# Optimization experiments

Hardware: AMD Instinct MI355X
Metric: run time of the kernel (lower is better)

## Reference

```python
import jax, jax.numpy as jnp
import numpy as np

D_MODEL, H, KV, HD = 2048, 32, 8, 64  # head_dim = 64, RoPE half-dim = 32
B, L = 2, 2048
EPS = 1e-06


def apply_rope(t, cos, sin):
    # t: [b,l,h,hd]; cos/sin: [1,l,1,hd//2] (broadcast over batch and heads)
    dim = t.shape[-1] // 2
    cos = cos[..., :dim]
    sin = sin[..., :dim]
    x1, x2 = t[..., :dim], t[..., dim:]
    return jnp.concatenate([x1 * cos - x2 * sin, x2 * cos + x1 * sin], axis=-1)


def setup_inputs() -> dict:
    key = jax.random.key(0)
    ks = jax.random.split(key, 5)
    x = jax.random.normal(ks[0], (B, L, D_MODEL), dtype=jnp.float32)
    # true rotary tables, theta=10000
    half = HD // 2
    inv_freq = 1.0 / (10000.0 ** (jnp.arange(half, dtype=jnp.float32) / half))
    ang = jnp.arange(L, dtype=jnp.float32)[:, None] * inv_freq[None, :]  # [L, half]
    cos = jnp.cos(ang)[None, :, None, :]  # [1,L,1,half]
    sin = jnp.sin(ang)[None, :, None, :]
    s = 0.02
    Wq = jax.random.normal(ks[1], (D_MODEL, D_MODEL), dtype=jnp.float32) * s
    Wk = jax.random.normal(ks[2], (D_MODEL, KV * HD), dtype=jnp.float32) * s
    Wv = jax.random.normal(ks[3], (D_MODEL, KV * HD), dtype=jnp.float32) * s
    Wo = jax.random.normal(ks[4], (D_MODEL, D_MODEL), dtype=jnp.float32) * s
    return {"x": x, "cos": cos, "sin": sin, "Wq": Wq, "Wk": Wk, "Wv": Wv, "Wo": Wo}


def reference(x, cos, sin, Wq, Wk, Wv, Wo):
    b, l, _ = x.shape
    q = (x @ Wq).reshape(b, l, H, HD)
    k = (x @ Wk).reshape(b, l, KV, HD)
    v = (x @ Wv).reshape(b, l, KV, HD)
    q = apply_rope(q, cos, sin)
    k = apply_rope(k, cos[:, :, :KV, :], sin[:, :, :KV, :])
    # QK RMS-norm (qk_norm=True path), done in fp32
    q32 = q.astype(jnp.float32)
    k32 = k.astype(jnp.float32)
    q = (q32 * jax.lax.rsqrt(jnp.mean(jnp.square(q32), axis=-1, keepdims=True) + EPS)).astype(q.dtype)
    k = (k32 * jax.lax.rsqrt(jnp.mean(jnp.square(k32), axis=-1, keepdims=True) + EPS)).astype(k.dtype)
    # GQA: repeat KV heads to match Q heads
    g = H // KV
    k = jnp.repeat(k, g, axis=2)
    v = jnp.repeat(v, g, axis=2)
    scale = jax.lax.rsqrt(jnp.float32(HD))
    scores = jnp.einsum('blhd,bmhd->bhlm', q, k) * scale  # [b,H,L,L]
    causal = jnp.tril(jnp.ones((l, l), dtype=jnp.bool_))[None, None]
    scores = jnp.where(causal, scores, jnp.full_like(scores, -10000.0))
    attn = jax.nn.softmax(scores.astype(jnp.float32), axis=-1).astype(v.dtype)
    out = jnp.einsum('bhql,blhd->bqhd', attn, v).reshape(b, l, D_MODEL)
    return out @ Wo
```

## Files before the change

### kernel.cpp

```cpp
#include <hip/hip_runtime.h>
#include <hip/hip_bf16.h>
#include <cstdint>
#include <cstddef>

#define D_MODEL 2048
#define NH 32
#define NKV 8
#define HD 64
#define BB 2
#define LL 2048
#define EPS 1e-6f
#define MM (BB * LL)
#define QS 3072
#define KO 2048
#define VO 2560

typedef __hip_bfloat16 bf16;
typedef short bf16x8 __attribute__((ext_vector_type(8)));
typedef short s16x4 __attribute__((ext_vector_type(4)));
typedef float f32x4 __attribute__((ext_vector_type(4)));

__device__ inline float4 ld_bf4u(const unsigned short* p) {
  const ushort4 u = *(const ushort4*)p;
  float4 r;
  r.x = __uint_as_float(((unsigned)u.x) << 16);
  r.y = __uint_as_float(((unsigned)u.y) << 16);
  r.z = __uint_as_float(((unsigned)u.z) << 16);
  r.w = __uint_as_float(((unsigned)u.w) << 16);
  return r;
}
__device__ inline float4 ld4_rt(const void* p, size_t i, bool f32) {
  if (f32) return *(const float4*)((const float*)p + i);
  return ld_bf4u((const unsigned short*)p + i);
}
__device__ inline float ld1_rt(const void* p, size_t i, bool f32) {
  if (f32) return ((const float*)p)[i];
  unsigned short u = ((const unsigned short*)p)[i];
  return __uint_as_float(((unsigned)u) << 16);
}
__device__ inline unsigned short f2bf(float f) {
  bf16 h = __float2bfloat16(f);
  return *reinterpret_cast<unsigned short*>(&h);
}
__device__ inline float bfu2f(unsigned short u) {
  return __uint_as_float(((unsigned)u) << 16);
}
__device__ inline void store1(float* p, float v) { *p = v; }
__device__ inline void store1(unsigned short* p, float v) { *p = f2bf(v); }

__device__ inline void glds16(const unsigned short* g, unsigned short* l) {
  __builtin_amdgcn_global_load_lds(
      (const __attribute__((address_space(1))) unsigned int*)g,
      (__attribute__((address_space(3))) unsigned int*)l, 16, 0, 0);
}

__global__ __launch_bounds__(256) void detect_all(
    const unsigned short* p0, const unsigned short* p1, const unsigned short* p2,
    const unsigned short* p3, const unsigned short* p4, const unsigned short* p5,
    const unsigned short* p6, int* __restrict__ flags) {
  const unsigned short* ptrs[7] = {p0, p1, p2, p3, p4, p5, p6};
  const int b = blockIdx.x;
  const uint4* p = (const uint4*)ptrs[b];
  __shared__ int found;
  if (threadIdx.x == 0) found = 0;
  __syncthreads();
  int loc = 0;
#pragma unroll
  for (int it = 0; it < 16; ++it) {
    uint4 v = p[it * 256 + threadIdx.x];
    unsigned wds[4] = {v.x, v.y, v.z, v.w};
#pragma unroll
    for (int q = 0; q < 4; ++q) {
      unsigned lo = wds[q] & 0xFFFFu, hi = wds[q] >> 16;
      if (((lo >> 7) & 0xFFu) == 0xFFu || ((hi >> 7) & 0xFFu) == 0xFFu) loc = 1;
    }
  }
  if (loc) atomicOr(&found, 1);
  __syncthreads();
  if (threadIdx.x == 0) flags[b] = found;
}

__global__ __launch_bounds__(256) void cvt_bf16(const void* __restrict__ src,
                                                unsigned short* __restrict__ dst,
                                                int n4, const int* __restrict__ flags, int idx) {
  const bool f32 = flags[idx] != 0;
  int i = blockIdx.x * 256 + threadIdx.x;
  if (i < n4) {
    float4 v = ld4_rt(src, (size_t)i * 4, f32);
    ushort4 o;
    o.x = f2bf(v.x); o.y = f2bf(v.y); o.z = f2bf(v.z); o.w = f2bf(v.w);
    *(ushort4*)&dst[(size_t)i * 4] = o;
  }
}

__global__ __launch_bounds__(256) void transpose_any(const void* __restrict__ src,
                                                     unsigned short* __restrict__ dst,
                                                     int K, int N,
                                                     const int* __restrict__ flags, int idx) {
  const bool f32 = flags[idx] != 0;
  __shared__ unsigned short tile[64][65];
  const int t = threadIdx.x;
  const int n0 = blockIdx.x * 64, k0 = blockIdx.y * 64;
  const int cr = t >> 4, cc = (t & 15) * 4;
#pragma unroll
  for (int rr = 0; rr < 4; ++rr) {
    int row = rr * 16 + cr;
    float4 v = ld4_rt(src, (size_t)(k0 + row) * N + n0 + cc, f32);
    tile[row][cc + 0] = f2bf(v.x);
    tile[row][cc + 1] = f2bf(v.y);
    tile[row][cc + 2] = f2bf(v.z);
    tile[row][cc + 3] = f2bf(v.w);
  }
  __syncthreads();
#pragma unroll
  for (int rr = 0; rr < 4; ++rr) {
    int nrow = rr * 16 + cr;
    ushort4 o;
    o.x = tile[cc + 0][nrow];
    o.y = tile[cc + 1][nrow];
    o.z = tile[cc + 2][nrow];
    o.w = tile[cc + 3][nrow];
    *(ushort4*)&dst[(size_t)(n0 + nrow) * K + k0 + cc] = o;
  }
}

__global__ __launch_bounds__(256) void v_to_vt(const unsigned short* __restrict__ qkv,
                                               unsigned short* __restrict__ vt) {
  __shared__ unsigned short tile[64][72];
  const int t = threadIdx.x;
  const int l0 = blockIdx.x * 64;
  const int bk = blockIdx.y;
  const int r = t >> 2, c16 = (t & 3) * 16;
  const int b = bk >> 3, kvh = bk & 7;
  const unsigned short* src = &qkv[(size_t)(b * LL + l0 + r) * QS + VO + kvh * 64 + c16];
  *(uint4*)&tile[r][c16] = *(const uint4*)&src[0];
  *(uint4*)&tile[r][c16 + 8] = *(const uint4*)&src[8];
  __syncthreads();
  unsigned short u[16];
#pragma unroll
  for (int j = 0; j < 16; ++j) u[j] = tile[c16 + j][r];
  unsigned short* dst = &vt[((size_t)bk * 64 + r) * LL + l0 + c16];
  *(uint4*)&dst[0] = *(uint4*)&u[0];
  *(uint4*)&dst[8] = *(uint4*)&u[8];
}

template <typename CT>
__global__ __launch_bounds__(256) void gemm_mfma(const unsigned short* __restrict__ A,
                                                 const unsigned short* __restrict__ Bt,
                                                 CT* __restrict__ C,
                                                 int M, int N, int K, int lda) {
  __shared__ __align__(16) unsigned short As[128 * 32];
  __shared__ __align__(16) unsigned short Bs[128 * 32];
  const int t = threadIdx.x;
  const int lane = t & 63, w = t >> 6;
  const int wm = (w >> 1) * 64, wn = (w & 1) * 64;
  const int g = lane >> 4, m16 = lane & 15;
  const int nwg = gridDim.x * gridDim.y;
  const int orig = blockIdx.y * gridDim.x + blockIdx.x;
  const int swz = (orig & 7) * (nwg >> 3) + (orig >> 3);
  const int m0 = (swz / gridDim.x) * 128, n0 = (swz % gridDim.x) * 128;
  const unsigned short* gA = &A[(size_t)(m0 + (t >> 2)) * lda + (t & 3) * 8];
  const unsigned short* gB = &Bt[(size_t)(n0 + (t >> 2)) * K + (t & 3) * 8];
  unsigned short* lA = &As[t * 8];
  unsigned short* lB = &Bs[t * 8];
  f32x4 acc[4][4] = {};
  for (int k0 = 0; k0 < K; k0 += 32) {
    __syncthreads();
    glds16(gA + k0, lA);
    glds16(gA + (size_t)64 * lda + k0, lA + 2048);
    glds16(gB + k0, lB);
    glds16(gB + (size_t)64 * K + k0, lB + 2048);
    __syncthreads();
    bf16x8 af[4], bfr[4];
#pragma unroll
    for (int i = 0; i < 4; ++i) af[i] = *(const bf16x8*)&As[(wm + i * 16 + m16) * 32 + g * 8];
#pragma unroll
    for (int j = 0; j < 4; ++j) bfr[j] = *(const bf16x8*)&Bs[(wn + j * 16 + m16) * 32 + g * 8];
#pragma unroll
    for (int i = 0; i < 4; ++i)
#pragma unroll
      for (int j = 0; j < 4; ++j)
        acc[i][j] = __builtin_amdgcn_mfma_f32_16x16x32_bf16(af[i], bfr[j], acc[i][j], 0, 0, 0);
  }
#pragma unroll
  for (int i = 0; i < 4; ++i)
#pragma unroll
    for (int j = 0; j < 4; ++j)
#pragma unroll
      for (int r = 0; r < 4; ++r) {
        int row = m0 + wm + i * 16 + g * 4 + r;
        int col = n0 + wn + j * 16 + m16;
        store1(&C[(size_t)row * N + col], acc[i][j][r]);
      }
}

__global__ __launch_bounds__(256) void rope_rms(unsigned short* __restrict__ qkv,
                                                const void* __restrict__ cosp,
                                                const void* __restrict__ sinp,
                                                const int* __restrict__ flags) {
  const bool cf = flags[1] != 0, sf = flags[2] != 0;
  const int wid = blockIdx.x * 4 + (threadIdx.x >> 6);
  const int lane = threadIdx.x & 63;
  const int hh = wid % (NH + NKV);
  const int bl = wid / (NH + NKV);
  const int l = bl & (LL - 1);
  unsigned short* base = (hh < NH) ? &qkv[(size_t)bl * QS + hh * 64]
                                   : &qkv[(size_t)bl * QS + KO + (hh - NH) * 64];
  const int j = lane & 31;
  float c = ld1_rt(cosp, l * 32 + j, cf);
  float s = ld1_rt(sinp, l * 32 + j, sf);
  float val = bfu2f(base[lane]);
  float other = __shfl_xor(val, 32);
  float r = (lane < 32) ? fmaf(val, c, -(other * s)) : fmaf(val, c, other * s);
  float ss = r * r;
#pragma unroll
  for (int off = 32; off; off >>= 1) ss += __shfl_xor(ss, off);
  base[lane] = f2bf(r * rsqrtf(ss * (1.0f / HD) + EPS));
}

__global__ __launch_bounds__(256) void attn_mfma(unsigned short* __restrict__ qkv,
                                                 const unsigned short* __restrict__ vt) {
  __shared__ __align__(16) unsigned short Ks[2][64 * 64];
  __shared__ __align__(16) unsigned short Vs[2][64 * 64];
  __shared__ __align__(16) unsigned short Pt[4][64 * 16];
  const int t = threadIdx.x, lane = t & 63, w = t >> 6;
  const int g = lane >> 4, m16 = lane & 15;
  const int h = blockIdx.x, b = blockIdx.y;
  const int qt = (LL / 64 - 1) - blockIdx.z;
  const int kvh = h >> 2;
  const int q0 = qt * 64, qr0 = q0 + w * 16;

  bf16x8 qf0, qf1;
  {
    const unsigned short* qrow = &qkv[(size_t)(b * LL + qr0 + m16) * QS + h * 64 + g * 8];
    qf0 = *(const bf16x8*)&qrow[0];
    qf1 = *(const bf16x8*)&qrow[32];
  }
  f32x4 Oacc[4] = {};
  float lrow[4] = {0.f, 0.f, 0.f, 0.f};

  const int lr = lane >> 3;
  const int lc = (lane & 7) ^ lr;
  const unsigned short* gK = &qkv[(size_t)(b * LL) * QS + KO + kvh * 64 + lc * 8];
  const unsigned short* gV = &vt[((size_t)(b * NKV + kvh) * 64 + w * 16 + lr) * LL + lc * 8];
  const int dbase = w * 1024 + lane * 8;
  const int nIter = q0 / 64 + 1;

#pragma unroll
  for (int c = 0; c < 2; ++c) {
    glds16(gK + (size_t)(w * 16 + c * 8 + lr) * QS, &Ks[0][dbase + c * 512]);
    glds16(gV + (size_t)c * 8 * LL, &Vs[0][dbase + c * 512]);
  }
  __syncthreads();

  const int sw8 = (m16 & 7) * 8;
  for (int it = 0; it < nIter; ++it) {
    const int j0 = it * 64;
    const int cur = it & 1;
    if (it + 1 < nIter) {
      const int nj = j0 + 64;
#pragma unroll
      for (int c = 0; c < 2; ++c) {
        glds16(gK + (size_t)(nj + w * 16 + c * 8 + lr) * QS, &Ks[cur ^ 1][dbase + c * 512]);
        glds16(gV + (size_t)c * 8 * LL + nj, &Vs[cur ^ 1][dbase + c * 512]);
      }
    }
    const unsigned short* KsB = Ks[cur];
    const unsigned short* VsB = Vs[cur];

    f32x4 S[4];
#pragma unroll
    for (int jt = 0; jt < 4; ++jt) {
      const int rb = (jt * 16 + m16) * 64;
      bf16x8 kf0 = *(const bf16x8*)&KsB[rb + ((g * 8) ^ sw8)];
      bf16x8 kf1 = *(const bf16x8*)&KsB[rb + (((g + 4) * 8) ^ sw8)];
      f32x4 z = {0.f, 0.f, 0.f, 0.f};
      z = __builtin_amdgcn_mfma_f32_16x16x32_bf16(qf0, kf0, z, 0, 0, 0);
      S[jt] = __builtin_amdgcn_mfma_f32_16x16x32_bf16(qf1, kf1, z, 0, 0, 0);
    }
    if (j0 == q0) {
#pragma unroll
      for (int jt = 0; jt < 4; ++jt)
#pragma unroll
        for (int r = 0; r < 4; ++r) {
          int col = q0 + jt * 16 + m16;
          int row = qr0 + g * 4 + r;
          float p = __expf(fmaf(S[jt][r], 0.125f, -8.0f));
          p = (col <= row) ? p : 0.f;
          S[jt][r] = p;
          lrow[r] += p;
        }
    } else {
#pragma unroll
      for (int jt = 0; jt < 4; ++jt)
#pragma unroll
        for (int r = 0; r < 4; ++r) {
          float p = __expf(fmaf(S[jt][r], 0.125f, -8.0f));
          S[jt][r] = p;
          lrow[r] += p;
        }
    }
#pragma unroll
    for (int jt = 0; jt < 4; ++jt) {
      ushort4 pw;
      pw.x = f2bf(S[jt][0]); pw.y = f2bf(S[jt][1]);
      pw.z = f2bf(S[jt][2]); pw.w = f2bf(S[jt][3]);
      *(ushort4*)&Pt[w][(jt * 16 + m16) * 16 + g * 4] = pw;
    }
    s16x4 a0, a1, b0, b1;
    {
      __attribute__((address_space(3))) unsigned short* p3 =
          (__attribute__((address_space(3))) unsigned short*)&Pt[w][g * 128 + m16 * 4];
      unsigned paddr = (unsigned)(size_t)p3;
      asm volatile(
          "s_waitcnt lgkmcnt(0)\n\t"
          "ds_read_b64_tr_b16 %0, %4\n\t"
          "ds_read_b64_tr_b16 %1, %4 offset:128\n\t"
          "ds_read_b64_tr_b16 %2, %4 offset:1024\n\t"
          "ds_read_b64_tr_b16 %3, %4 offset:1152\n\t"
          "s_waitcnt lgkmcnt(0)"
          : "=&v"(a0), "=&v"(a1), "=&v"(b0), "=&v"(b1)
          : "v"(paddr)
          : "memory");
      __builtin_amdgcn_sched_barrier(0);
    }
    bf16x8 pf0 = __builtin_shufflevector(a0, a1, 0, 1, 2, 3, 4, 5, 6, 7);
    bf16x8 pf1 = __builtin_shufflevector(b0, b1, 0, 1, 2, 3, 4, 5, 6, 7);
#pragma unroll
    for (int dt = 0; dt < 4; ++dt) {
      const int rb = (dt * 16 + m16) * 64;
      bf16x8 vf0 = *(const bf16x8*)&VsB[rb + ((g * 8) ^ sw8)];
      bf16x8 vf1 = *(const bf16x8*)&VsB[rb + (((g + 4) * 8) ^ sw8)];
      Oacc[dt] = __builtin_amdgcn_mfma_f32_16x16x32_bf16(pf0, vf0, Oacc[dt], 0, 0, 0);
      Oacc[dt] = __builtin_amdgcn_mfma_f32_16x16x32_bf16(pf1, vf1, Oacc[dt], 0, 0, 0);
    }
    __syncthreads();
  }
  float inv[4];
#pragma unroll
  for (int r = 0; r < 4; ++r) {
#pragma unroll
    for (int off = 1; off < 16; off <<= 1) lrow[r] += __shfl_xor(lrow[r], off);
    inv[r] = 1.0f / lrow[r];
  }
#pragma unroll
  for (int dt = 0; dt < 4; ++dt)
#pragma unroll
    for (int r = 0; r < 4; ++r) {
      int row = qr0 + g * 4 + r;
      qkv[(size_t)(b * LL + row) * QS + h * 64 + dt * 16 + m16] = f2bf(Oacc[dt][r] * inv[r]);
    }
}

extern "C" void kernel_launch(void* const* d_in, const int* in_sizes, int n_in,
                              void* d_out, int out_size, void* d_ws, size_t ws_size,
                              hipStream_t stream) {
  const void* x = d_in[0];
  const void* cosp = d_in[1];
  const void* sinp = d_in[2];
  const void* Wq = d_in[3];
  const void* Wk = d_in[4];
  const void* Wv = d_in[5];
  const void* Wo = d_in[6];
  float* out = (float*)d_out;

  char* w0 = (char*)d_ws;
  int* flags = (int*)w0;
  unsigned short* xb = (unsigned short*)(w0 + 256);
  unsigned short* qkvb = xb + (size_t)MM * 2048;
  unsigned short* WqkvT = qkvb + (size_t)MM * QS;
  unsigned short* WoT = WqkvT + (size_t)QS * 2048;
  unsigned short* vt = WoT + (size_t)2048 * 2048;

  detect_all<<<7, 256, 0, stream>>>(
      (const unsigned short*)x, (const unsigned short*)cosp, (const unsigned short*)sinp,
      (const unsigned short*)Wq, (const unsigned short*)Wk, (const unsigned short*)Wv,
      (const unsigned short*)Wo, flags);
  cvt_bf16<<<MM * 2048 / 4 / 256, 256, 0, stream>>>(x, xb, MM * 2048 / 4, flags, 0);
  transpose_any<<<dim3(2048 / 64, 2048 / 64), 256, 0, stream>>>(Wq, WqkvT, 2048, 2048, flags, 3);
  transpose_any<<<dim3(512 / 64, 2048 / 64), 256, 0, stream>>>(Wk, WqkvT + (size_t)KO * 2048, 2048, 512, flags, 4);
  transpose_any<<<dim3(512 / 64, 2048 / 64), 256, 0, stream>>>(Wv, WqkvT + (size_t)VO * 2048, 2048, 512, flags, 5);
  transpose_any<<<dim3(2048 / 64, 2048 / 64), 256, 0, stream>>>(Wo, WoT, 2048, 2048, flags, 6);
  gemm_mfma<unsigned short><<<dim3(QS / 128, MM / 128), 256, 0, stream>>>(xb, WqkvT, qkvb, MM, QS, 2048, 2048);
  rope_rms<<<MM * (NH + NKV) / 4, 256, 0, stream>>>(qkvb, cosp, sinp, flags);
  v_to_vt<<<dim3(LL / 64, BB * NKV), 256, 0, stream>>>(qkvb, vt);
  attn_mfma<<<dim3(NH, BB, LL / 64), 256, 0, stream>>>(qkvb, vt);
  gemm_mfma<float><<<dim3(2048 / 128, MM / 128), 256, 0, stream>>>(qkvb, WoT, out, MM, 2048, 2048, QS);
}
```

Measured before the change: 350.6 us.

## Fuse RoPE and QK RMS-norm into QKV GEMM epilogue; double-buffer GEMM LDS

Removes the separate rope_rms kernel by applying rotary embedding and per-head RMS normalization directly on the GEMM accumulators before storing Q/K columns. This saves a full read/write pass over the Q/K activations and one launch. The GEMM also gains double-buffered shared-memory tiles so the next K-slice is loaded while MFMAs run on the current one. This doubles LDS use, which may reduce occupancy.

New measurement: 338.2 us. 3.6% less time.

```diff
diff --git a/kernel.cpp b/kernel.cpp
--- a/kernel.cpp
+++ b/kernel.cpp
@@ -144,13 +144,16 @@
   *(uint4*)&dst[8] = *(uint4*)&u[8];
 }
 
-template <typename CT>
+template <typename CT, int FUSE>
 __global__ __launch_bounds__(256) void gemm_mfma(const unsigned short* __restrict__ A,
                                                  const unsigned short* __restrict__ Bt,
                                                  CT* __restrict__ C,
-                                                 int M, int N, int K, int lda) {
-  __shared__ __align__(16) unsigned short As[128 * 32];
-  __shared__ __align__(16) unsigned short Bs[128 * 32];
+                                                 int M, int N, int K, int lda,
+                                                 const void* __restrict__ cosp,
+                                                 const void* __restrict__ sinp,
+                                                 const int* __restrict__ flags) {
+  __shared__ __align__(16) unsigned short As[2][128 * 32];
+  __shared__ __align__(16) unsigned short Bs[2][128 * 32];
   const int t = threadIdx.x;
   const int lane = t & 63, w = t >> 6;
   const int wm = (w >> 1) * 64, wn = (w & 1) * 64;
@@ -161,26 +164,66 @@
   const int m0 = (swz / gridDim.x) * 128, n0 = (swz % gridDim.x) * 128;
   const unsigned short* gA = &A[(size_t)(m0 + (t >> 2)) * lda + (t & 3) * 8];
   const unsigned short* gB = &Bt[(size_t)(n0 + (t >> 2)) * K + (t & 3) * 8];
-  unsigned short* lA = &As[t * 8];
-  unsigned short* lB = &Bs[t * 8];
+  const int l8 = t * 8;
   f32x4 acc[4][4] = {};
+  glds16(gA, &As[0][l8]);
+  glds16(gA + (size_t)64 * lda, &As[0][l8 + 2048]);
+  glds16(gB, &Bs[0][l8]);
+  glds16(gB + (size_t)64 * K, &Bs[0][l8 + 2048]);
+  __syncthreads();
+  int cur = 0;
   for (int k0 = 0; k0 < K; k0 += 32) {
-    __syncthreads();
-    glds16(gA + k0, lA);
-    glds16(gA + (size_t)64 * lda + k0, lA + 2048);
-    glds16(gB + k0, lB);
-    glds16(gB + (size_t)64 * K + k0, lB + 2048);
-    __syncthreads();
+    if (k0 + 32 < K) {
+      glds16(gA + k0 + 32, &As[cur ^ 1][l8]);
+      glds16(gA + (size_t)64 * lda + k0 + 32, &As[cur ^ 1][l8 + 2048]);
+      glds16(gB + k0 + 32, &Bs[cur ^ 1][l8]);
+      glds16(gB + (size_t)64 * K + k0 + 32, &Bs[cur ^ 1][l8 + 2048]);
+    }
     bf16x8 af[4], bfr[4];
 #pragma unroll
-    for (int i = 0; i < 4; ++i) af[i] = *(const bf16x8*)&As[(wm + i * 16 + m16) * 32 + g * 8];
-#pragma unroll
-    for (int j = 0; j < 4; ++j) bfr[j] = *(const bf16x8*)&Bs[(wn + j * 16 + m16) * 32 + g * 8];
+    for (int i = 0; i < 4; ++i) af[i] = *(const bf16x8*)&As[cur][(wm + i * 16 + m16) * 32 + g * 8];
+#pragma unroll
+    for (int j = 0; j < 4; ++j) bfr[j] = *(const bf16x8*)&Bs[cur][(wn + j * 16 + m16) * 32 + g * 8];
 #pragma unroll
     for (int i = 0; i < 4; ++i)
 #pragma unroll
       for (int j = 0; j < 4; ++j)
         acc[i][j] = __builtin_amdgcn_mfma_f32_16x16x32_bf16(af[i], bfr[j], acc[i][j], 0, 0, 0);
+    __syncthreads();
+    cur ^= 1;
+  }
+  if constexpr (FUSE) {
+    const int colbase = n0 + wn;
+    if (colbase < VO) {
+      const bool cf = flags[1] != 0, sf = flags[2] != 0;
+#pragma unroll
+      for (int i = 0; i < 4; ++i)
+#pragma unroll
+        for (int r = 0; r < 4; ++r) {
+          const int row = m0 + wm + i * 16 + g * 4 + r;
+          const int l = row & (LL - 1);
+          const float c0 = ld1_rt(cosp, l * 32 + m16, cf);
+          const float c1 = ld1_rt(cosp, l * 32 + 16 + m16, cf);
+          const float s0 = ld1_rt(sinp, l * 32 + m16, sf);
+          const float s1 = ld1_rt(sinp, l * 32 + 16 + m16, sf);
+          const float x0 = acc[i][0][r], x1 = acc[i][1][r];
+          const float x2 = acc[i][2][r], x3 = acc[i][3][r];
+          const float r0 = x0 * c0 - x2 * s0;
+          const float r1 = x1 * c1 - x3 * s1;
+          const float r2 = x2 * c0 + x0 * s0;
+          const float r3 = x3 * c1 + x1 * s1;
+          float ss = r0 * r0 + r1 * r1 + r2 * r2 + r3 * r3;
+#pragma unroll
+          for (int off = 1; off < 16; off <<= 1) ss += __shfl_xor(ss, off);
+          const float sc = rsqrtf(ss * (1.0f / HD) + EPS);
+          CT* cr = &C[(size_t)row * N + colbase + m16];
+          store1(cr + 0, r0 * sc);
+          store1(cr + 16, r1 * sc);
+          store1(cr + 32, r2 * sc);
+          store1(cr + 48, r3 * sc);
+        }
+      return;
+    }
   }
 #pragma unroll
   for (int i = 0; i < 4; ++i)
@@ -192,30 +235,6 @@
         int col = n0 + wn + j * 16 + m16;
         store1(&C[(size_t)row * N + col], acc[i][j][r]);
       }
-}
-
-__global__ __launch_bounds__(256) void rope_rms(unsigned short* __restrict__ qkv,
-                                                const void* __restrict__ cosp,
-                                                const void* __restrict__ sinp,
-                                                const int* __restrict__ flags) {
-  const bool cf = flags[1] != 0, sf = flags[2] != 0;
-  const int wid = blockIdx.x * 4 + (threadIdx.x >> 6);
-  const int lane = threadIdx.x & 63;
-  const int hh = wid % (NH + NKV);
-  const int bl = wid / (NH + NKV);
-  const int l = bl & (LL - 1);
-  unsigned short* base = (hh < NH) ? &qkv[(size_t)bl * QS + hh * 64]
-                                   : &qkv[(size_t)bl * QS + KO + (hh - NH) * 64];
-  const int j = lane & 31;
-  float c = ld1_rt(cosp, l * 32 + j, cf);
-  float s = ld1_rt(sinp, l * 32 + j, sf);
-  float val = bfu2f(base[lane]);
-  float other = __shfl_xor(val, 32);
-  float r = (lane < 32) ? fmaf(val, c, -(other * s)) : fmaf(val, c, other * s);
-  float ss = r * r;
-#pragma unroll
-  for (int off = 32; off; off >>= 1) ss += __shfl_xor(ss, off);
-  base[lane] = f2bf(r * rsqrtf(ss * (1.0f / HD) + EPS));
 }
 
 __global__ __launch_bounds__(256) void attn_mfma(unsigned short* __restrict__ qkv,
@@ -381,9 +400,10 @@
   transpose_any<<<dim3(512 / 64, 2048 / 64), 256, 0, stream>>>(Wk, WqkvT + (size_t)KO * 2048, 2048, 512, flags, 4);
   transpose_any<<<dim3(512 / 64, 2048 / 64), 256, 0, stream>>>(Wv, WqkvT + (size_t)VO * 2048, 2048, 512, flags, 5);
   transpose_any<<<dim3(2048 / 64, 2048 / 64), 256, 0, stream>>>(Wo, WoT, 2048, 2048, flags, 6);
-  gemm_mfma<unsigned short><<<dim3(QS / 128, MM / 128), 256, 0, stream>>>(xb, WqkvT, qkvb, MM, QS, 2048, 2048);
-  rope_rms<<<MM * (NH + NKV) / 4, 256, 0, stream>>>(qkvb, cosp, sinp, flags);
+  gemm_mfma<unsigned short, 1><<<dim3(QS / 128, MM / 128), 256, 0, stream>>>(
+      xb, WqkvT, qkvb, MM, QS, 2048, 2048, cosp, sinp, flags);
   v_to_vt<<<dim3(LL / 64, BB * NKV), 256, 0, stream>>>(qkvb, vt);
   attn_mfma<<<dim3(NH, BB, LL / 64), 256, 0, stream>>>(qkvb, vt);
-  gemm_mfma<float><<<dim3(2048 / 128, MM / 128), 256, 0, stream>>>(qkvb, WoT, out, MM, 2048, 2048, QS);
-}
+  gemm_mfma<float, 0><<<dim3(2048 / 128, MM / 128), 256, 0, stream>>>(
+      qkvb, WoT, out, MM, 2048, 2048, QS, nullptr, nullptr, nullptr);
+}
```
